# Kernel optimization log

Measured on AMD Instinct MI355X. Metric: run time of the kernel, lower is better.

The kernel has to match this reference:

```python
import jax, jax.numpy as jnp
import numpy as np

EMBED = 768
HEADS = 12
HEAD_DIM = EMBED // HEADS


def setup_inputs() -> dict:
    key = jax.random.key(0)
    ks = jax.random.split(key, 9)
    B, S, E = 2, 2048, EMBED
    sc = 1.0 / np.sqrt(E)
    return {
        "x": jax.random.normal(ks[0], (B, S, E), dtype=jnp.float32),
        "Wq": jax.random.normal(ks[1], (E, E), dtype=jnp.float32) * sc,
        "bq": jnp.zeros((E,), dtype=jnp.float32),
        "Wk": jax.random.normal(ks[2], (E, E), dtype=jnp.float32) * sc,
        "bk": jnp.zeros((E,), dtype=jnp.float32),
        "Wv": jax.random.normal(ks[3], (E, E), dtype=jnp.float32) * sc,
        "bv": jnp.zeros((E,), dtype=jnp.float32),
        "Wo": jax.random.normal(ks[4], (E, E), dtype=jnp.float32) * sc,
        "bo": jnp.zeros((E,), dtype=jnp.float32),
    }


def _split_heads(t):
    B, S, E = t.shape
    return t.reshape(B, S, HEADS, HEAD_DIM).transpose(0, 2, 1, 3)  # [B,H,S,D]


def reference(x, Wq, bq, Wk, bk, Wv, bv, Wo, bo):
    B, S, E = x.shape
    Q = _split_heads(x @ Wq + bq)
    K = _split_heads(x @ Wk + bk)
    V = _split_heads(x @ Wv + bv)
    scale = 1.0 / jnp.sqrt(jnp.asarray(HEAD_DIM, dtype=x.dtype))
    scores = jnp.einsum("bhqd,bhkd->bhqk", Q, K) * scale  # [B,H,S,S]
    attn_weights = jax.nn.softmax(scores, axis=-1)
    attn = jnp.einsum("bhqk,bhkd->bhqd", attn_weights, V)  # [B,H,S,D]
    attn = attn.transpose(0, 2, 1, 3).reshape(B, S, E)
    out = attn @ Wo + bo
    return out, attn_weights
```

## Files before the change

### kernel.cpp

```cpp
#include <hip/hip_runtime.h>
#include <cstddef>

#define B_ 2
#define S_ 2048
#define E_ 768
#define H_ 12
#define D_ 64
#define M_ (B_*S_)

typedef float f4 __attribute__((ext_vector_type(4)));
typedef short short8 __attribute__((ext_vector_type(8)));

__device__ __forceinline__ short f2bf(float f) {
    union { float f; unsigned u; } v; v.f = f;
    unsigned r = (v.u + 0x7fffu + ((v.u >> 16) & 1u)) >> 16;
    return (short)r;
}

__device__ __forceinline__ void stage64(const short* __restrict__ g0, int rstride,
                                        short8* lds, int w, int lane)
{
    #pragma unroll
    for (int i = 0; i < 2; ++i) {
        const int n = w * 128 + i * 64 + lane;
        const int r = n >> 3, s = n & 7;
        const int cc = s ^ (r & 7);
        const short* src = g0 + (size_t)r * rstride + cc * 8;
        __builtin_amdgcn_global_load_lds(
            (const __attribute__((address_space(1))) unsigned int*)src,
            (__attribute__((address_space(3))) unsigned int*)(lds + w * 128 + i * 64),
            16, 0, 0);
    }
}

__global__ __launch_bounds__(256) void cvt_bf16_k(const float* __restrict__ in,
                                                  short* __restrict__ out, int n8)
{
    int i = blockIdx.x * 256 + threadIdx.x;
    if (i >= n8) return;
    f4 a = *(const f4*)(in + (size_t)i * 8);
    f4 b = *(const f4*)(in + (size_t)i * 8 + 4);
    short8 o;
    o[0] = f2bf(a[0]); o[1] = f2bf(a[1]); o[2] = f2bf(a[2]); o[3] = f2bf(a[3]);
    o[4] = f2bf(b[0]); o[5] = f2bf(b[1]); o[6] = f2bf(b[2]); o[7] = f2bf(b[3]);
    *(short8*)(out + (size_t)i * 8) = o;
}

__global__ __launch_bounds__(256) void wtrans_k(const float* __restrict__ Wq,
                                                const float* __restrict__ Wk,
                                                const float* __restrict__ Wv,
                                                const float* __restrict__ Wo,
                                                short* __restrict__ Wt)
{
    __shared__ float T[32][33];
    const float* W = (blockIdx.z == 0) ? Wq : (blockIdx.z == 1) ? Wk
                   : (blockIdx.z == 2) ? Wv : Wo;
    short* o = Wt + (size_t)blockIdx.z * E_ * E_;
    const int tx = threadIdx.x & 31, ty = threadIdx.x >> 5;
    const int k0 = blockIdx.y * 32, n0 = blockIdx.x * 32;
    #pragma unroll
    for (int i = 0; i < 4; ++i)
        T[ty * 4 + i][tx] = W[(size_t)(k0 + ty * 4 + i) * E_ + n0 + tx];
    __syncthreads();
    #pragma unroll
    for (int i = 0; i < 4; ++i)
        o[(size_t)(n0 + ty * 4 + i) * E_ + k0 + tx] = f2bf(T[tx][ty * 4 + i]);
}

template<int MODE>
__global__ __launch_bounds__(256) void gemm_mfma_k(
    const short* __restrict__ A, const short* __restrict__ Bt,
    const float* __restrict__ bias, float* __restrict__ outf,
    short* __restrict__ outb, float scale)
{
    __shared__ short8 As[2][64][8];
    __shared__ short8 Bs[2][64][8];
    const int t = threadIdx.x;
    const int w = t >> 6, lane = t & 63, ln = lane & 15, quad = lane >> 4;
    const int m0 = blockIdx.y * 64, n0 = blockIdx.x * 64;

    const short* Ab = A  + (size_t)m0 * E_;
    const short* Bb = Bt + (size_t)n0 * E_;

    f4 acc[4];
    #pragma unroll
    for (int i = 0; i < 4; ++i) acc[i] = (f4){0.f, 0.f, 0.f, 0.f};

    stage64(Ab, E_, &As[0][0][0], w, lane);
    stage64(Bb, E_, &Bs[0][0][0], w, lane);
    __syncthreads();

    int cb = 0;
    for (int k0 = 0; k0 < E_; k0 += 64) {
        if (k0 + 64 < E_) {
            stage64(Ab + k0 + 64, E_, &As[cb ^ 1][0][0], w, lane);
            stage64(Bb + k0 + 64, E_, &Bs[cb ^ 1][0][0], w, lane);
        }
        const int ar = w * 16 + ln;
        short8 af0 = As[cb][ar][quad ^ (ar & 7)];
        short8 af1 = As[cb][ar][(quad + 4) ^ (ar & 7)];
        #pragma unroll
        for (int ng = 0; ng < 4; ++ng) {
            int br = ng * 16 + ln;
            short8 bf0 = Bs[cb][br][quad ^ (br & 7)];
            short8 bf1 = Bs[cb][br][(quad + 4) ^ (br & 7)];
            acc[ng] = __builtin_amdgcn_mfma_f32_16x16x32_bf16(af0, bf0, acc[ng], 0, 0, 0);
            acc[ng] = __builtin_amdgcn_mfma_f32_16x16x32_bf16(af1, bf1, acc[ng], 0, 0, 0);
        }
        __syncthreads();
        cb ^= 1;
    }

    #pragma unroll
    for (int ng = 0; ng < 4; ++ng) {
        int c = n0 + ng * 16 + ln;
        float bv = bias[c];
        #pragma unroll
        for (int g = 0; g < 4; ++g) {
            int r = m0 + w * 16 + quad * 4 + g;
            float v = acc[ng][g] + bv;
            if (MODE == 0) {
                outf[(size_t)r * E_ + c] = v;
            } else {
                int b = r >> 11, s = r & (S_ - 1);
                int h = c >> 6,  d = c & (D_ - 1);
                if (MODE == 1)
                    outb[((size_t)(b * H_ + h) * S_ + s) * D_ + d] = f2bf(v * scale);
                else
                    outb[((size_t)(b * H_ + h) * D_ + d) * S_ + s] = f2bf(v);
            }
        }
    }
}

__global__ __launch_bounds__(256) void attn_k(
    const short* __restrict__ Qb, const short* __restrict__ Kb,
    const short* __restrict__ Vt, float* __restrict__ P,
    short* __restrict__ ctxb)
{
    __shared__ short8 KT[2][64][8];
    __shared__ short8 VT[2][64][8];
    __shared__ short  PT[4][16][72];

    const int t    = threadIdx.x;
    const int w    = t >> 6;
    const int lane = t & 63, ln = lane & 15, quad = lane >> 4;
    const int bh   = blockIdx.y;
    const int qr   = blockIdx.x * 64 + w * 16;

    const size_t kvbase = (size_t)bh * S_ * D_;
    const short* Kbase = Kb + kvbase;
    const short* Vbase = Vt + kvbase;

    short8 qf0, qf1;
    {
        const short* qrow = Qb + kvbase + (size_t)(qr + ln) * D_;
        qf0 = *(const short8*)(qrow + quad * 8);
        qf1 = *(const short8*)(qrow + 32 + quad * 8);
    }

    f4 l_acc = {0.f, 0.f, 0.f, 0.f};

    stage64(Kbase, D_, &KT[0][0][0], w, lane);
    __syncthreads();
    int cb = 0;
    for (int k0 = 0; k0 < S_; k0 += 64) {
        if (k0 + 64 < S_)
            stage64(Kbase + (size_t)(k0 + 64) * D_, D_, &KT[cb ^ 1][0][0], w, lane);
        #pragma unroll
        for (int kg = 0; kg < 4; ++kg) {
            int row = kg * 16 + ln;
            short8 kf0 = KT[cb][row][quad ^ (row & 7)];
            short8 kf1 = KT[cb][row][(quad + 4) ^ (row & 7)];
            f4 sc = {0.f, 0.f, 0.f, 0.f};
            sc = __builtin_amdgcn_mfma_f32_16x16x32_bf16(qf0, kf0, sc, 0, 0, 0);
            sc = __builtin_amdgcn_mfma_f32_16x16x32_bf16(qf1, kf1, sc, 0, 0, 0);
            #pragma unroll
            for (int g = 0; g < 4; ++g) l_acc[g] += __expf(sc[g] - 8.0f);
        }
        __syncthreads();
        cb ^= 1;
    }

    f4 inv_l;
    #pragma unroll
    for (int g = 0; g < 4; ++g) {
        float v = l_acc[g];
        v += __shfl_xor(v, 1, 64);
        v += __shfl_xor(v, 2, 64);
        v += __shfl_xor(v, 4, 64);
        v += __shfl_xor(v, 8, 64);
        inv_l[g] = 1.0f / v;
    }

    f4 acc[4];
    #pragma unroll
    for (int dg = 0; dg < 4; ++dg) acc[dg] = (f4){0.f, 0.f, 0.f, 0.f};

    float* Pw = P + ((size_t)bh * S_ + qr) * S_;

    stage64(Kbase, D_, &KT[0][0][0], w, lane);
    stage64(Vbase, S_, &VT[0][0][0], w, lane);
    __syncthreads();
    cb = 0;
    for (int k0 = 0; k0 < S_; k0 += 64) {
        if (k0 + 64 < S_) {
            stage64(Kbase + (size_t)(k0 + 64) * D_, D_, &KT[cb ^ 1][0][0], w, lane);
            stage64(Vbase + k0 + 64,                S_, &VT[cb ^ 1][0][0], w, lane);
        }
        #pragma unroll
        for (int kg = 0; kg < 4; ++kg) {
            int row = kg * 16 + ln;
            short8 kf0 = KT[cb][row][quad ^ (row & 7)];
            short8 kf1 = KT[cb][row][(quad + 4) ^ (row & 7)];
            f4 sc = {0.f, 0.f, 0.f, 0.f};
            sc = __builtin_amdgcn_mfma_f32_16x16x32_bf16(qf0, kf0, sc, 0, 0, 0);
            sc = __builtin_amdgcn_mfma_f32_16x16x32_bf16(qf1, kf1, sc, 0, 0, 0);
            #pragma unroll
            for (int g = 0; g < 4; ++g) {
                float p = __expf(sc[g] - 8.0f) * inv_l[g];
                Pw[(size_t)(quad * 4 + g) * S_ + k0 + kg * 16 + ln] = p;
                PT[w][quad * 4 + g][kg * 16 + ln] = f2bf(p);
            }
        }
        short8 af0 = *(const short8*)&PT[w][ln][quad * 8];
        short8 af1 = *(const short8*)&PT[w][ln][32 + quad * 8];
        #pragma unroll
        for (int dg = 0; dg < 4; ++dg) {
            int row = dg * 16 + ln;
            short8 vf0 = VT[cb][row][quad ^ (row & 7)];
            short8 vf1 = VT[cb][row][(quad + 4) ^ (row & 7)];
            acc[dg] = __builtin_amdgcn_mfma_f32_16x16x32_bf16(af0, vf0, acc[dg], 0, 0, 0);
            acc[dg] = __builtin_amdgcn_mfma_f32_16x16x32_bf16(af1, vf1, acc[dg], 0, 0, 0);
        }
        __syncthreads();
        cb ^= 1;
    }

    const int b = bh / H_, h = bh % H_;
    #pragma unroll
    for (int dg = 0; dg < 4; ++dg)
        #pragma unroll
        for (int g = 0; g < 4; ++g)
            ctxb[(size_t)(b * S_ + qr + quad * 4 + g) * E_ + h * D_ + dg * 16 + ln]
                = f2bf(acc[dg][g]);
}

extern "C" void kernel_launch(void* const* d_in, const int* in_sizes, int n_in,
                              void* d_out, int out_size, void* d_ws, size_t ws_size,
                              hipStream_t stream) {
    const float* x  = (const float*)d_in[0];
    const float* Wq = (const float*)d_in[1];
    const float* bq = (const float*)d_in[2];
    const float* Wk = (const float*)d_in[3];
    const float* bk = (const float*)d_in[4];
    const float* Wv = (const float*)d_in[5];
    const float* bv = (const float*)d_in[6];
    const float* Wo = (const float*)d_in[7];
    const float* bo = (const float*)d_in[8];

    const size_t NE = (size_t)M_ * E_;
    const size_t W2 = (size_t)E_ * E_;
    short* xb  = (short*)d_ws;
    short* Wt  = xb + NE;
    short* Qb  = Wt + 4 * W2;
    short* Kb  = Qb + NE;
    short* Vtb = Kb + NE;
    short* Cb  = Vtb + NE;

    float* out0  = (float*)d_out;
    float* attnw = out0 + NE;

    cvt_bf16_k<<<dim3((int)(NE / 8 / 256)), 256, 0, stream>>>(x, xb, (int)(NE / 8));
    wtrans_k<<<dim3(24, 24, 4), 256, 0, stream>>>(Wq, Wk, Wv, Wo, Wt);

    dim3 gg(E_ / 64, M_ / 64);
    gemm_mfma_k<1><<<gg, 256, 0, stream>>>(xb, Wt + 0 * W2, bq, nullptr, Qb, 0.125f);
    gemm_mfma_k<1><<<gg, 256, 0, stream>>>(xb, Wt + 1 * W2, bk, nullptr, Kb, 1.0f);
    gemm_mfma_k<2><<<gg, 256, 0, stream>>>(xb, Wt + 2 * W2, bv, nullptr, Vtb, 1.0f);
    attn_k<<<dim3(S_ / 64, B_ * H_), 256, 0, stream>>>(Qb, Kb, Vtb, attnw, Cb);
    gemm_mfma_k<0><<<gg, 256, 0, stream>>>(Cb, Wt + 3 * W2, bo, out0, nullptr, 1.0f);
}
```

Measured before the change: 563.3 us.

## Load K/V fragments directly from global and transpose score MFMA for vectorized P stores

New measurement: 702.1 us. 24.6% more time.

```diff
diff --git a/kernel.cpp b/kernel.cpp
--- a/kernel.cpp
+++ b/kernel.cpp
@@ -9,6 +9,7 @@
 #define M_ (B_*S_)
 
 typedef float f4 __attribute__((ext_vector_type(4)));
+typedef short short4v __attribute__((ext_vector_type(4)));
 typedef short short8 __attribute__((ext_vector_type(8)));
 
 __device__ __forceinline__ short f2bf(float f) {
@@ -138,9 +139,7 @@
     const short* __restrict__ Vt, float* __restrict__ P,
     short* __restrict__ ctxb)
 {
-    __shared__ short8 KT[2][64][8];
-    __shared__ short8 VT[2][64][8];
-    __shared__ short  PT[4][16][72];
+    __shared__ short PT[4][16][72];
 
     const int t    = threadIdx.x;
     const int w    = t >> 6;
@@ -149,8 +148,8 @@
     const int qr   = blockIdx.x * 64 + w * 16;
 
     const size_t kvbase = (size_t)bh * S_ * D_;
-    const short* Kbase = Kb + kvbase;
-    const short* Vbase = Vt + kvbase;
+    const short* Kp = Kb + kvbase;
+    const short* Vp = Vt + kvbase;
 
     short8 qf0, qf1;
     {
@@ -159,82 +158,58 @@
         qf1 = *(const short8*)(qrow + 32 + quad * 8);
     }
 
-    f4 l_acc = {0.f, 0.f, 0.f, 0.f};
-
-    stage64(Kbase, D_, &KT[0][0][0], w, lane);
-    __syncthreads();
-    int cb = 0;
+    float l_acc = 0.f;
     for (int k0 = 0; k0 < S_; k0 += 64) {
-        if (k0 + 64 < S_)
-            stage64(Kbase + (size_t)(k0 + 64) * D_, D_, &KT[cb ^ 1][0][0], w, lane);
         #pragma unroll
         for (int kg = 0; kg < 4; ++kg) {
-            int row = kg * 16 + ln;
-            short8 kf0 = KT[cb][row][quad ^ (row & 7)];
-            short8 kf1 = KT[cb][row][(quad + 4) ^ (row & 7)];
+            const short* krow = Kp + (size_t)(k0 + kg * 16 + ln) * D_;
+            short8 kf0 = *(const short8*)(krow + quad * 8);
+            short8 kf1 = *(const short8*)(krow + 32 + quad * 8);
             f4 sc = {0.f, 0.f, 0.f, 0.f};
-            sc = __builtin_amdgcn_mfma_f32_16x16x32_bf16(qf0, kf0, sc, 0, 0, 0);
-            sc = __builtin_amdgcn_mfma_f32_16x16x32_bf16(qf1, kf1, sc, 0, 0, 0);
+            sc = __builtin_amdgcn_mfma_f32_16x16x32_bf16(kf0, qf0, sc, 0, 0, 0);
+            sc = __builtin_amdgcn_mfma_f32_16x16x32_bf16(kf1, qf1, sc, 0, 0, 0);
             #pragma unroll
-            for (int g = 0; g < 4; ++g) l_acc[g] += __expf(sc[g] - 8.0f);
-        }
-        __syncthreads();
-        cb ^= 1;
-    }
-
-    f4 inv_l;
-    #pragma unroll
-    for (int g = 0; g < 4; ++g) {
-        float v = l_acc[g];
-        v += __shfl_xor(v, 1, 64);
-        v += __shfl_xor(v, 2, 64);
-        v += __shfl_xor(v, 4, 64);
-        v += __shfl_xor(v, 8, 64);
-        inv_l[g] = 1.0f / v;
-    }
+            for (int g = 0; g < 4; ++g) l_acc += __expf(sc[g] - 8.0f);
+        }
+    }
+    l_acc += __shfl_xor(l_acc, 16, 64);
+    l_acc += __shfl_xor(l_acc, 32, 64);
+    const float inv_l = 1.0f / l_acc;
 
     f4 acc[4];
     #pragma unroll
     for (int dg = 0; dg < 4; ++dg) acc[dg] = (f4){0.f, 0.f, 0.f, 0.f};
 
-    float* Pw = P + ((size_t)bh * S_ + qr) * S_;
-
-    stage64(Kbase, D_, &KT[0][0][0], w, lane);
-    stage64(Vbase, S_, &VT[0][0][0], w, lane);
-    __syncthreads();
-    cb = 0;
+    float* Pw = P + ((size_t)bh * S_ + qr + ln) * S_;
+
     for (int k0 = 0; k0 < S_; k0 += 64) {
-        if (k0 + 64 < S_) {
-            stage64(Kbase + (size_t)(k0 + 64) * D_, D_, &KT[cb ^ 1][0][0], w, lane);
-            stage64(Vbase + k0 + 64,                S_, &VT[cb ^ 1][0][0], w, lane);
-        }
         #pragma unroll
         for (int kg = 0; kg < 4; ++kg) {
-            int row = kg * 16 + ln;
-            short8 kf0 = KT[cb][row][quad ^ (row & 7)];
-            short8 kf1 = KT[cb][row][(quad + 4) ^ (row & 7)];
+            const short* krow = Kp + (size_t)(k0 + kg * 16 + ln) * D_;
+            short8 kf0 = *(const short8*)(krow + quad * 8);
+            short8 kf1 = *(const short8*)(krow + 32 + quad * 8);
             f4 sc = {0.f, 0.f, 0.f, 0.f};
-            sc = __builtin_amdgcn_mfma_f32_16x16x32_bf16(qf0, kf0, sc, 0, 0, 0);
-            sc = __builtin_amdgcn_mfma_f32_16x16x32_bf16(qf1, kf1, sc, 0, 0, 0);
+            sc = __builtin_amdgcn_mfma_f32_16x16x32_bf16(kf0, qf0, sc, 0, 0, 0);
+            sc = __builtin_amdgcn_mfma_f32_16x16x32_bf16(kf1, qf1, sc, 0, 0, 0);
+            f4 p; short4v pb;
             #pragma unroll
             for (int g = 0; g < 4; ++g) {
-                float p = __expf(sc[g] - 8.0f) * inv_l[g];
-                Pw[(size_t)(quad * 4 + g) * S_ + k0 + kg * 16 + ln] = p;
-                PT[w][quad * 4 + g][kg * 16 + ln] = f2bf(p);
+                p[g]  = __expf(sc[g] - 8.0f) * inv_l;
+                pb[g] = f2bf(p[g]);
             }
+            *(f4*)(Pw + k0 + kg * 16 + quad * 4) = p;
+            *(short4v*)&PT[w][ln][kg * 16 + quad * 4] = pb;
         }
         short8 af0 = *(const short8*)&PT[w][ln][quad * 8];
         short8 af1 = *(const short8*)&PT[w][ln][32 + quad * 8];
         #pragma unroll
         for (int dg = 0; dg < 4; ++dg) {
-            int row = dg * 16 + ln;
-            short8 vf0 = VT[cb][row][quad ^ (row & 7)];
-            short8 vf1 = VT[cb][row][(quad + 4) ^ (row & 7)];
+            const short* vrow = Vp + (size_t)(dg * 16 + ln) * S_ + k0;
+            short8 vf0 = *(const short8*)(vrow + quad * 8);
+            short8 vf1 = *(const short8*)(vrow + 32 + quad * 8);
             acc[dg] = __builtin_amdgcn_mfma_f32_16x16x32_bf16(af0, vf0, acc[dg], 0, 0, 0);
             acc[dg] = __builtin_amdgcn_mfma_f32_16x16x32_bf16(af1, vf1, acc[dg], 0, 0, 0);
         }
-        __syncthreads();
-        cb ^= 1;
     }
 
     const int b = bh / H_, h = bh % H_;
```
